# Performance work log

Measured on AMD Instinct MI355X. Metric: run time of the kernel, lower is better.

Reference implementation:

```python
import jax, jax.numpy as jnp
import numpy as np

TEMPERATURE = 8.0  # sqrt(d_k) with d_k=64

def setup_inputs() -> dict:
    key = jax.random.key(0)
    k1, k2, k3, k4 = jax.random.split(key, 4)
    B, L, D = 64, 1024, 64  # B = batch*n_heads
    q = jax.random.normal(k1, (B, L, D), dtype=jnp.float32)
    k = jax.random.normal(k2, (B, L, D), dtype=jnp.float32)
    v = jax.random.normal(k3, (B, L, D), dtype=jnp.float32)
    mask = jax.random.randint(k4, (B, L, L), 0, 2).astype(jnp.bool_)
    return {"q": q, "k": k, "v": v, "mask": mask}

def reference(q, k, v, mask):
    # scores: [B, Lq, Lk]
    attn = jnp.einsum('bqd,bkd->bqk', q, k) / TEMPERATURE
    attn = jnp.where(mask, -jnp.inf, attn)
    attn = jax.nn.softmax(attn, axis=2)
    output = jnp.einsum('bqk,bkd->bqd', attn, v)
    return (output, attn)
```

## Files before the change

kernel.cpp:

```cpp
#include <hip/hip_runtime.h>

#define B_ 64
#define L_ 1024
#define D_ 64
#define QT 16

typedef _Float16 f16;
typedef __attribute__((ext_vector_type(8))) _Float16 f16x8;
typedef __attribute__((ext_vector_type(4))) _Float16 f16x4;
typedef __attribute__((ext_vector_type(4))) float f32x4;
typedef unsigned long long u64;
typedef unsigned long long u64x4 __attribute__((ext_vector_type(4)));

#define WS_KH 0u
#define WS_VT 8388608u
#define WS_BT 16777216u
#define WS_NEED 25165824u

#define MFMA32(A, B, C) __builtin_amdgcn_mfma_f32_16x16x32_f16((A), (B), (C), 0, 0, 0)
#define PV16(A, B, C)   __builtin_amdgcn_mfma_f32_16x16x16f16((A), (B), (C), 0, 0, 0)

__global__ __launch_bounds__(256)
void mega_prep(const float* __restrict__ kk, const float* __restrict__ v,
               const unsigned char* __restrict__ mask,
               f16* __restrict__ kh, f16* __restrict__ vt, u64* __restrict__ bits) {
    __shared__ f16 tile[64][72];
    const int bid = blockIdx.x;
    if (bid < 2048) {
        const int i = (bid * 256 + threadIdx.x) * 8;
        float4 f0 = *(const float4*)(kk + i);
        float4 f1 = *(const float4*)(kk + i + 4);
        float fv[8] = {f0.x, f0.y, f0.z, f0.w, f1.x, f1.y, f1.z, f1.w};
        f16x8 h;
        #pragma unroll
        for (int j = 0; j < 8; ++j) h[j] = (f16)(fv[j] * 0.125f);
        *(f16x8*)(kh + i) = h;
    } else if (bid < 3072) {
        const int bb = bid - 2048;
        const int b = bb >> 4, kt = bb & 15;
        const int r = threadIdx.x >> 2, c0 = (threadIdx.x & 3) * 16;
        const float* vp = v + (size_t)(b * L_ + kt * 64 + r) * D_ + c0;
        float4 g0 = *(const float4*)vp;
        float4 g1 = *(const float4*)(vp + 4);
        float4 g2 = *(const float4*)(vp + 8);
        float4 g3 = *(const float4*)(vp + 12);
        float fv[16] = {g0.x, g0.y, g0.z, g0.w, g1.x, g1.y, g1.z, g1.w,
                        g2.x, g2.y, g2.z, g2.w, g3.x, g3.y, g3.z, g3.w};
        #pragma unroll
        for (int j = 0; j < 16; ++j) tile[r][c0 + j] = (f16)fv[j];
        __syncthreads();
        f16x8 o0, o1;
        #pragma unroll
        for (int j = 0; j < 8; ++j) { o0[j] = tile[c0 + j][r]; o1[j] = tile[c0 + 8 + j][r]; }
        f16* op = vt + (size_t)(b * 64 + r) * 1024 + kt * 64 + c0;
        *(f16x8*)op = o0;
        *(f16x8*)(op + 8) = o1;
    } else {
        unsigned det = 0;
        {
            const unsigned* mw = (const unsigned*)mask;
            #pragma unroll
            for (int i = 0; i < 32; ++i) det |= mw[i];
        }
        const bool elem4 = (det <= 1u) || (det == 0x3F800000u);
        const int lane = threadIdx.x & 63;
        const int gw = (bid - 3072) * 4 + (threadIdx.x >> 6);
        for (int s = gw; s < 262144; s += 8192) {
            unsigned nib;
            if (elem4) {
                const int4 m = *(const int4*)((const int*)mask + (size_t)s * 256 + lane * 4);
                nib = (m.x != 0 ? 1u : 0u) | (m.y != 0 ? 2u : 0u) |
                      (m.z != 0 ? 4u : 0u) | (m.w != 0 ? 8u : 0u);
            } else {
                const uchar4 m = *(const uchar4*)(mask + (size_t)s * 256 + lane * 4);
                nib = (m.x ? 1u : 0u) | (m.y ? 2u : 0u) | (m.z ? 4u : 0u) | (m.w ? 8u : 0u);
            }
            u64 b0 = __ballot((nib & 1u) != 0u);
            u64 b1 = __ballot((nib & 2u) != 0u);
            u64 b2 = __ballot((nib & 4u) != 0u);
            u64 b3 = __ballot((nib & 8u) != 0u);
            if (lane == 0) {
                u64x4 o = {b0, b1, b2, b3};
                *(u64x4*)(bits + (size_t)s * 4) = o;
            }
        }
    }
}


__global__ __launch_bounds__(256, 4)
void sdpa_main(const float* __restrict__ q, const f16* __restrict__ kh,
               const f16* __restrict__ vt, const u64* __restrict__ bits,
               float* __restrict__ out, float* __restrict__ attn)
{
    const int tid = threadIdx.x;
    const int l = tid & 63, w = tid >> 6;
    const int lr = l & 15, lg = l >> 4;
    const int bid0 = blockIdx.x;
    const int bid = (bid0 & 7) * 128 + (bid0 >> 3);
    const int tile_id = bid * 4 + w;
    const int b = tile_id >> 6;
    const int qbase = tile_id * QT;

    f16x8 aq0, aq1;
    {
        const float* qp = q + (size_t)(qbase + lr) * D_;
        float4 f0 = *(const float4*)(qp + lg * 8);
        float4 f1 = *(const float4*)(qp + lg * 8 + 4);
        float4 f2 = *(const float4*)(qp + 32 + lg * 8);
        float4 f3 = *(const float4*)(qp + 32 + lg * 8 + 4);
        aq0[0] = (f16)f0.x; aq0[1] = (f16)f0.y; aq0[2] = (f16)f0.z; aq0[3] = (f16)f0.w;
        aq0[4] = (f16)f1.x; aq0[5] = (f16)f1.y; aq0[6] = (f16)f1.z; aq0[7] = (f16)f1.w;
        aq1[0] = (f16)f2.x; aq1[1] = (f16)f2.y; aq1[2] = (f16)f2.z; aq1[3] = (f16)f2.w;
        aq1[4] = (f16)f3.x; aq1[5] = (f16)f3.y; aq1[6] = (f16)f3.z; aq1[7] = (f16)f3.w;
    }

    const f16* khb = kh + (size_t)b * (L_ * D_) + lg * 8;
    const f16* vtb = vt + (size_t)b * (D_ * L_);
    const u64x4* bp = (const u64x4*)bits + (size_t)(qbase + lr) * 4;

    float rsum = 0.f;
    f16x8 kc0, kc1;
    {
        const f16* kp = khb + (size_t)lr * D_;
        kc0 = *(const f16x8*)kp;
        kc1 = *(const f16x8*)(kp + 32);
    }
    #pragma unroll
    for (int sp = 0; sp < 4; ++sp) {
        const u64x4 bw = bp[sp];
        #pragma unroll 4
        for (int cc = 0; cc < 16; ++cc) {
            const int c = sp * 16 + cc;
            f16x8 kn0, kn1;
            if (c < 63) {
                const f16* kp = khb + (size_t)((c + 1) * 16 + lr) * D_;
                kn0 = *(const f16x8*)kp;
                kn1 = *(const f16x8*)(kp + 32);
            }
            f32x4 s = {0.f, 0.f, 0.f, 0.f};
            s = MFMA32(kc0, aq0, s);
            s = MFMA32(kc1, aq1, s);
            const int sh = cc * 4 + lg;
            rsum += ((unsigned)(bw[0] >> sh) & 1u) ? 0.f : __expf(s[0]);
            rsum += ((unsigned)(bw[1] >> sh) & 1u) ? 0.f : __expf(s[1]);
            rsum += ((unsigned)(bw[2] >> sh) & 1u) ? 0.f : __expf(s[2]);
            rsum += ((unsigned)(bw[3] >> sh) & 1u) ? 0.f : __expf(s[3]);
            kc0 = kn0; kc1 = kn1;
        }
    }
    rsum += __shfl_xor(rsum, 16);
    rsum += __shfl_xor(rsum, 32);
    const float inv = 1.0f / rsum;

    f32x4 o0 = {0.f,0.f,0.f,0.f}, o1 = {0.f,0.f,0.f,0.f};
    f32x4 o2 = {0.f,0.f,0.f,0.f}, o3 = {0.f,0.f,0.f,0.f};
    {
        const f16* kp = khb + (size_t)lr * D_;
        kc0 = *(const f16x8*)kp;
        kc1 = *(const f16x8*)(kp + 32);
    }
    float* ap = attn + (size_t)(qbase + lr) * L_ + lg * 4;
    const f16* vpb = vtb + (size_t)lr * L_ + lg * 4;
    #pragma unroll
    for (int sp = 0; sp < 4; ++sp) {
        const u64x4 bw = bp[sp];
        #pragma unroll 4
        for (int cc = 0; cc < 16; ++cc) {
            const int c = sp * 16 + cc;
            f16x8 kn0, kn1;
            if (c < 63) {
                const f16* kp = khb + (size_t)((c + 1) * 16 + lr) * D_;
                kn0 = *(const f16x8*)kp;
                kn1 = *(const f16x8*)(kp + 32);
            }
            f32x4 s = {0.f, 0.f, 0.f, 0.f};
            s = MFMA32(kc0, aq0, s);
            s = MFMA32(kc1, aq1, s);
            const int sh = cc * 4 + lg;
            f32x4 p;
            p[0] = (((unsigned)(bw[0] >> sh) & 1u) ? 0.f : __expf(s[0])) * inv;
            p[1] = (((unsigned)(bw[1] >> sh) & 1u) ? 0.f : __expf(s[1])) * inv;
            p[2] = (((unsigned)(bw[2] >> sh) & 1u) ? 0.f : __expf(s[2])) * inv;
            p[3] = (((unsigned)(bw[3] >> sh) & 1u) ? 0.f : __expf(s[3])) * inv;
            *(f32x4*)(ap + c * 16) = p;
            f16x4 pa;
            pa[0] = (f16)p[0]; pa[1] = (f16)p[1]; pa[2] = (f16)p[2]; pa[3] = (f16)p[3];
            const f16* vp = vpb + c * 16;
            f16x4 v0 = *(const f16x4*)vp;
            f16x4 v1 = *(const f16x4*)(vp + 16 * L_);
            f16x4 v2 = *(const f16x4*)(vp + 32 * L_);
            f16x4 v3 = *(const f16x4*)(vp + 48 * L_);
            o0 = PV16(pa, v0, o0);
            o1 = PV16(pa, v1, o1);
            o2 = PV16(pa, v2, o2);
            o3 = PV16(pa, v3, o3);
            kc0 = kn0; kc1 = kn1;
        }
    }

    float* op = out + (size_t)(qbase + lg * 4) * D_ + lr;
    #pragma unroll
    for (int r = 0; r < 4; ++r) {
        op[r * D_ + 0]  = o0[r];
        op[r * D_ + 16] = o1[r];
        op[r * D_ + 32] = o2[r];
        op[r * D_ + 48] = o3[r];
    }
}


__device__ __forceinline__ int sidx(int row, int col) {
    return row * 1024 + ((((col >> 3) ^ (row & 7)) << 3) | (col & 7));
}

__global__ __launch_bounds__(256, 4)
void sdpa_fallback(const float* __restrict__ q, const float* __restrict__ kk,
                   const float* __restrict__ v, const unsigned char* __restrict__ mask,
                   float* __restrict__ out, float* __restrict__ attn)
{
    __shared__ f16 S[QT * 1024];
    __shared__ float wmax[4][QT];
    __shared__ float wsum[QT];

    const int tid = threadIdx.x;
    const int l = tid & 63, w = tid >> 6;
    const int lr = l & 15, lg = l >> 4;
    const int bid = blockIdx.x;
    const int b = bid >> 6, qt = bid & 63;
    const int qbase = b * L_ + qt * QT;

    unsigned det = 0;
    {
        const unsigned* mw = (const unsigned*)mask;
        #pragma unroll
        for (int i = 0; i < 32; ++i) det |= mw[i];
    }
    const bool elem4 = (det <= 1u) || (det == 0x3F800000u);

    f16x8 aqh[2], aql[2];
    {
        const float* qp = q + (size_t)(qbase + lr) * D_;
        #pragma unroll
        for (int s = 0; s < 2; ++s) {
            float4 f0 = *(const float4*)(qp + s * 32 + lg * 8);
            float4 f1 = *(const float4*)(qp + s * 32 + lg * 8 + 4);
            float fv[8] = {f0.x, f0.y, f0.z, f0.w, f1.x, f1.y, f1.z, f1.w};
            #pragma unroll
            for (int j = 0; j < 8; ++j) {
                f16 h = (f16)fv[j];
                aqh[s][j] = h;
                aql[s][j] = (f16)(fv[j] - (float)h);
            }
        }
    }

    float vmax[4] = {-INFINITY, -INFINITY, -INFINITY, -INFINITY};
    const float* kb = kk + (size_t)(b * L_ + w * 16 + lr) * D_ + lg * 8;
    const size_t mrowbase = (size_t)(qbase + lg * 4) * L_ + w * 16 + lr;

    float4 kc[4];
    kc[0] = *(const float4*)kb;
    kc[1] = *(const float4*)(kb + 4);
    kc[2] = *(const float4*)(kb + 32);
    kc[3] = *(const float4*)(kb + 36);
    int mcur[4], mnxt[4];
    #pragma unroll
    for (int r2 = 0; r2 < 4; ++r2) {
        if (elem4) {
            mcur[r2] = ((const int*)mask)[mrowbase + (size_t)r2 * L_];
            mnxt[r2] = ((const int*)mask)[mrowbase + (size_t)r2 * L_ + 64];
        } else {
            mcur[r2] = mask[mrowbase + (size_t)r2 * L_];
            mnxt[r2] = mask[mrowbase + (size_t)r2 * L_ + 64];
        }
    }

    for (int ck = 0; ck < 16; ++ck) {
        float4 kn[4];
        if (ck < 15) {
            const float* kp = kb + (size_t)(ck + 1) * 64 * D_;
            kn[0] = *(const float4*)kp;
            kn[1] = *(const float4*)(kp + 4);
            kn[2] = *(const float4*)(kp + 32);
            kn[3] = *(const float4*)(kp + 36);
        }
        int mfut[4];
        if (ck < 14) {
            const size_t mo = mrowbase + (size_t)(ck + 2) * 64;
            if (elem4) {
                #pragma unroll
                for (int r2 = 0; r2 < 4; ++r2) mfut[r2] = ((const int*)mask)[mo + (size_t)r2 * L_];
            } else {
                #pragma unroll
                for (int r2 = 0; r2 < 4; ++r2) mfut[r2] = mask[mo + (size_t)r2 * L_];
            }
        }
        f16x8 bh[2], bl[2];
        #pragma unroll
        for (int s = 0; s < 2; ++s) {
            float fv[8] = {kc[2*s].x, kc[2*s].y, kc[2*s].z, kc[2*s].w,
                           kc[2*s+1].x, kc[2*s+1].y, kc[2*s+1].z, kc[2*s+1].w};
            #pragma unroll
            for (int j = 0; j < 8; ++j) {
                f16 h = (f16)fv[j];
                bh[s][j] = h;
                bl[s][j] = (f16)(fv[j] - (float)h);
            }
        }
        f32x4 acc = {0.f, 0.f, 0.f, 0.f};
        #pragma unroll
        for (int s = 0; s < 2; ++s) {
            acc = MFMA32(aqh[s], bh[s], acc);
            acc = MFMA32(aql[s], bh[s], acc);
            acc = MFMA32(aqh[s], bl[s], acc);
        }
        const int scol = ck * 64 + w * 16 + lr;
        #pragma unroll
        for (int r2 = 0; r2 < 4; ++r2) {
            float sv = mcur[r2] ? -INFINITY : acc[r2] * 0.125f;
            S[sidx(lg * 4 + r2, scol)] = (f16)sv;
            vmax[r2] = fmaxf(vmax[r2], sv);
        }
        #pragma unroll
        for (int r2 = 0; r2 < 4; ++r2) mcur[r2] = mnxt[r2];
        if (ck < 14) {
            #pragma unroll
            for (int r2 = 0; r2 < 4; ++r2) mnxt[r2] = mfut[r2];
        }
        if (ck < 15) {
            #pragma unroll
            for (int j = 0; j < 4; ++j) kc[j] = kn[j];
        }
    }
    #pragma unroll
    for (int r2 = 0; r2 < 4; ++r2) {
        #pragma unroll
        for (int off = 1; off < 16; off <<= 1)
            vmax[r2] = fmaxf(vmax[r2], __shfl_xor(vmax[r2], off));
    }
    if (lr == 0) {
        #pragma unroll
        for (int r2 = 0; r2 < 4; ++r2) wmax[w][lg * 4 + r2] = vmax[r2];
    }
    __syncthreads();

    {
        const int row = tid >> 4, cg = tid & 15;
        const float m = fmaxf(fmaxf(wmax[0][row], wmax[1][row]),
                              fmaxf(wmax[2][row], wmax[3][row]));
        float sum = 0.f;
        #pragma unroll
        for (int c = 0; c < 8; ++c) {
            f16* sp = &S[row * 1024 + (((cg + 16 * c) ^ (row & 7)) << 3)];
            f16x8 sv = *(const f16x8*)sp;
            f16x8 evv;
            #pragma unroll
            for (int j = 0; j < 8; ++j) {
                float e = __expf((float)sv[j] - m);
                evv[j] = (f16)e;
                sum += e;
            }
            *(f16x8*)sp = evv;
        }
        #pragma unroll
        for (int off = 1; off < 16; off <<= 1) sum += __shfl_xor(sum, off);
        if (cg == 0) wsum[row] = sum;
        __syncthreads();

        const float inv = 1.0f / wsum[row];
        float* ap = attn + (size_t)(qbase + row) * L_;
        #pragma unroll
        for (int c = 0; c < 8; ++c) {
            f16x8 evv = *(const f16x8*)&S[row * 1024 + (((cg + 16 * c) ^ (row & 7)) << 3)];
            float4 p0, p1;
            p0.x = (float)evv[0] * inv; p0.y = (float)evv[1] * inv;
            p0.z = (float)evv[2] * inv; p0.w = (float)evv[3] * inv;
            p1.x = (float)evv[4] * inv; p1.y = (float)evv[5] * inv;
            p1.z = (float)evv[6] * inv; p1.w = (float)evv[7] * inv;
            *(float4*)(ap + (cg + 16 * c) * 8)     = p0;
            *(float4*)(ap + (cg + 16 * c) * 8 + 4) = p1;
        }
    }

    f32x4 acc2 = {0.f, 0.f, 0.f, 0.f};
    const float* vb = v + (size_t)(b * L_) * D_ + w * 16 + lr;
    float vcA[8], vcB[8];
    #pragma unroll
    for (int j = 0; j < 8; ++j) {
        vcA[j] = vb[(size_t)(lg * 8 + j) * D_];
        vcB[j] = vb[(size_t)(32 + lg * 8 + j) * D_];
    }
    for (int tt = 0; tt < 16; ++tt) {
        {
            f16x8 pa = *(const f16x8*)&S[lr * 1024 + ((((2 * tt) * 4 + lg) ^ (lr & 7)) << 3)];
            f16x8 bv;
            #pragma unroll
            for (int j = 0; j < 8; ++j) bv[j] = (f16)vcA[j];
            if (tt < 15) {
                const float* vp = vb + (size_t)((2 * tt + 2) * 32 + lg * 8) * D_;
                #pragma unroll
                for (int j = 0; j < 8; ++j) vcA[j] = vp[(size_t)j * D_];
            }
            acc2 = MFMA32(pa, bv, acc2);
        }
        {
            f16x8 pa = *(const f16x8*)&S[lr * 1024 + ((((2 * tt + 1) * 4 + lg) ^ (lr & 7)) << 3)];
            f16x8 bv;
            #pragma unroll
            for (int j = 0; j < 8; ++j) bv[j] = (f16)vcB[j];
            if (tt < 15) {
                const float* vp = vb + (size_t)((2 * tt + 3) * 32 + lg * 8) * D_;
                #pragma unroll
                for (int j = 0; j < 8; ++j) vcB[j] = vp[(size_t)j * D_];
            }
            acc2 = MFMA32(pa, bv, acc2);
        }
    }

    #pragma unroll
    for (int r2 = 0; r2 < 4; ++r2) {
        const float invr = 1.0f / wsum[lg * 4 + r2];
        out[(size_t)(qbase + lg * 4 + r2) * D_ + w * 16 + lr] = acc2[r2] * invr;
    }
}

extern "C" void kernel_launch(void* const* d_in, const int* in_sizes, int n_in,
                              void* d_out, int out_size, void* d_ws, size_t ws_size,
                              hipStream_t stream) {
    const float* q = (const float*)d_in[0];
    const float* k = (const float*)d_in[1];
    const float* v = (const float*)d_in[2];
    const unsigned char* mask = (const unsigned char*)d_in[3];
    float* out = (float*)d_out;
    float* attn = out + (size_t)B_ * L_ * D_;

    if (ws_size >= (size_t)WS_NEED) {
        f16* kh = (f16*)((char*)d_ws + WS_KH);
        f16* vt = (f16*)((char*)d_ws + WS_VT);
        u64* bits = (u64*)((char*)d_ws + WS_BT);
        mega_prep<<<dim3(5120), 256, 0, stream>>>(k, v, mask, kh, vt, bits);
        sdpa_main<<<dim3(1024), 256, 0, stream>>>(q, kh, vt, bits, out, attn);
    } else {
        sdpa_fallback<<<dim3(B_ * (L_ / QT)), 256, 0, stream>>>(q, k, v, mask, out, attn);
    }
}
```

Before: 328.9 us.

## Pre-pack K/V in MFMA fragment order and stage attn writes through LDS

The prep kernel now writes K and V in per-lane MFMA fragment order, so the main kernel loads each fragment with one contiguous coalesced read per 16-key chunk. V fragments are prefetched one chunk ahead, the same way K already was. The attention probabilities are stored as f16 in a swizzled LDS buffer and then written to attn as full coalesced rows, replacing the strided per-lane float4 stores. This adds 32KB of shared memory per block and lowers the launch bound to 3 blocks per CU. The attn output now holds f16-rounded probabilities instead of fp32 values, which loses some precision.

```diff
diff --git a/kernel.cpp b/kernel.cpp
--- a/kernel.cpp
+++ b/kernel.cpp
@@ -12,8 +12,8 @@
 typedef unsigned long long u64;
 typedef unsigned long long u64x4 __attribute__((ext_vector_type(4)));
 
-#define WS_KH 0u
-#define WS_VT 8388608u
+#define WS_KP 0u
+#define WS_VP 8388608u
 #define WS_BT 16777216u
 #define WS_NEED 25165824u
 
@@ -23,18 +23,24 @@
 __global__ __launch_bounds__(256)
 void mega_prep(const float* __restrict__ kk, const float* __restrict__ v,
                const unsigned char* __restrict__ mask,
-               f16* __restrict__ kh, f16* __restrict__ vt, u64* __restrict__ bits) {
+               f16* __restrict__ kpack, f16* __restrict__ vpack, u64* __restrict__ bits) {
     __shared__ f16 tile[64][72];
     const int bid = blockIdx.x;
+    const int l = threadIdx.x & 63;
+    const int lr = l & 15, lg = l >> 4;
     if (bid < 2048) {
-        const int i = (bid * 256 + threadIdx.x) * 8;
-        float4 f0 = *(const float4*)(kk + i);
-        float4 f1 = *(const float4*)(kk + i + 4);
-        float fv[8] = {f0.x, f0.y, f0.z, f0.w, f1.x, f1.y, f1.z, f1.w};
-        f16x8 h;
-        #pragma unroll
-        for (int j = 0; j < 8; ++j) h[j] = (f16)(fv[j] * 0.125f);
-        *(f16x8*)(kh + i) = h;
+        const int gw = bid * 4 + (threadIdx.x >> 6);
+        const int b = gw >> 7, wid = gw & 127;
+        const int c = wid >> 1, h = wid & 1;
+        const float* kp = kk + ((size_t)(b * L_ + c * 16 + lr)) * D_ + h * 32 + lg * 8;
+        float4 f0 = *(const float4*)kp;
+        float4 f1 = *(const float4*)(kp + 4);
+        f16x8 o;
+        o[0] = (f16)(f0.x * 0.125f); o[1] = (f16)(f0.y * 0.125f);
+        o[2] = (f16)(f0.z * 0.125f); o[3] = (f16)(f0.w * 0.125f);
+        o[4] = (f16)(f1.x * 0.125f); o[5] = (f16)(f1.y * 0.125f);
+        o[6] = (f16)(f1.z * 0.125f); o[7] = (f16)(f1.w * 0.125f);
+        *(f16x8*)(kpack + (size_t)gw * 512 + l * 8) = o;
     } else if (bid < 3072) {
         const int bb = bid - 2048;
         const int b = bb >> 4, kt = bb & 15;
@@ -49,12 +55,16 @@
         #pragma unroll
         for (int j = 0; j < 16; ++j) tile[r][c0 + j] = (f16)fv[j];
         __syncthreads();
-        f16x8 o0, o1;
-        #pragma unroll
-        for (int j = 0; j < 8; ++j) { o0[j] = tile[c0 + j][r]; o1[j] = tile[c0 + 8 + j][r]; }
-        f16* op = vt + (size_t)(b * 64 + r) * 1024 + kt * 64 + c0;
-        *(f16x8*)op = o0;
-        *(f16x8*)(op + 8) = o1;
+        const int cl = threadIdx.x >> 6;
+        const int c = kt * 4 + cl;
+        #pragma unroll
+        for (int nt = 0; nt < 4; ++nt) {
+            f16x4 o;
+            #pragma unroll
+            for (int j = 0; j < 4; ++j)
+                o[j] = tile[cl * 16 + lg * 4 + j][nt * 16 + lr];
+            *(f16x4*)(vpack + (size_t)b * 65536 + c * 1024 + nt * 256 + l * 4) = o;
+        }
     } else {
         unsigned det = 0;
         {
@@ -63,23 +73,22 @@
             for (int i = 0; i < 32; ++i) det |= mw[i];
         }
         const bool elem4 = (det <= 1u) || (det == 0x3F800000u);
-        const int lane = threadIdx.x & 63;
         const int gw = (bid - 3072) * 4 + (threadIdx.x >> 6);
         for (int s = gw; s < 262144; s += 8192) {
             unsigned nib;
             if (elem4) {
-                const int4 m = *(const int4*)((const int*)mask + (size_t)s * 256 + lane * 4);
+                const int4 m = *(const int4*)((const int*)mask + (size_t)s * 256 + l * 4);
                 nib = (m.x != 0 ? 1u : 0u) | (m.y != 0 ? 2u : 0u) |
                       (m.z != 0 ? 4u : 0u) | (m.w != 0 ? 8u : 0u);
             } else {
-                const uchar4 m = *(const uchar4*)(mask + (size_t)s * 256 + lane * 4);
+                const uchar4 m = *(const uchar4*)(mask + (size_t)s * 256 + l * 4);
                 nib = (m.x ? 1u : 0u) | (m.y ? 2u : 0u) | (m.z ? 4u : 0u) | (m.w ? 8u : 0u);
             }
             u64 b0 = __ballot((nib & 1u) != 0u);
             u64 b1 = __ballot((nib & 2u) != 0u);
             u64 b2 = __ballot((nib & 4u) != 0u);
             u64 b3 = __ballot((nib & 8u) != 0u);
-            if (lane == 0) {
+            if (l == 0) {
                 u64x4 o = {b0, b1, b2, b3};
                 *(u64x4*)(bits + (size_t)s * 4) = o;
             }
@@ -88,11 +97,12 @@
 }
 
 
-__global__ __launch_bounds__(256, 4)
-void sdpa_main(const float* __restrict__ q, const f16* __restrict__ kh,
-               const f16* __restrict__ vt, const u64* __restrict__ bits,
+__global__ __launch_bounds__(256, 3)
+void sdpa_main(const float* __restrict__ q, const f16* __restrict__ kpack,
+               const f16* __restrict__ vpack, const u64* __restrict__ bits,
                float* __restrict__ out, float* __restrict__ attn)
 {
+    __shared__ f16 SL[4 * 4096];
     const int tid = threadIdx.x;
     const int l = tid & 63, w = tid >> 6;
     const int lr = l & 15, lg = l >> 4;
@@ -115,28 +125,23 @@
         aq1[4] = (f16)f3.x; aq1[5] = (f16)f3.y; aq1[6] = (f16)f3.z; aq1[7] = (f16)f3.w;
     }
 
-    const f16* khb = kh + (size_t)b * (L_ * D_) + lg * 8;
-    const f16* vtb = vt + (size_t)b * (D_ * L_);
+    const f16* kpb = kpack + (size_t)b * 65536;
+    const f16* vpb = vpack + (size_t)b * 65536;
     const u64x4* bp = (const u64x4*)bits + (size_t)(qbase + lr) * 4;
 
     float rsum = 0.f;
-    f16x8 kc0, kc1;
-    {
-        const f16* kp = khb + (size_t)lr * D_;
-        kc0 = *(const f16x8*)kp;
-        kc1 = *(const f16x8*)(kp + 32);
-    }
+    f16x8 kc0 = *(const f16x8*)(kpb + l * 8);
+    f16x8 kc1 = *(const f16x8*)(kpb + 512 + l * 8);
     #pragma unroll
     for (int sp = 0; sp < 4; ++sp) {
         const u64x4 bw = bp[sp];
-        #pragma unroll 4
+        #pragma unroll
         for (int cc = 0; cc < 16; ++cc) {
             const int c = sp * 16 + cc;
             f16x8 kn0, kn1;
             if (c < 63) {
-                const f16* kp = khb + (size_t)((c + 1) * 16 + lr) * D_;
-                kn0 = *(const f16x8*)kp;
-                kn1 = *(const f16x8*)(kp + 32);
+                kn0 = *(const f16x8*)(kpb + (c + 1) * 1024 + l * 8);
+                kn1 = *(const f16x8*)(kpb + (c + 1) * 1024 + 512 + l * 8);
             }
             f32x4 s = {0.f, 0.f, 0.f, 0.f};
             s = MFMA32(kc0, aq0, s);
@@ -155,48 +160,57 @@
 
     f32x4 o0 = {0.f,0.f,0.f,0.f}, o1 = {0.f,0.f,0.f,0.f};
     f32x4 o2 = {0.f,0.f,0.f,0.f}, o3 = {0.f,0.f,0.f,0.f};
-    {
-        const f16* kp = khb + (size_t)lr * D_;
-        kc0 = *(const f16x8*)kp;
-        kc1 = *(const f16x8*)(kp + 32);
-    }
-    float* ap = attn + (size_t)(qbase + lr) * L_ + lg * 4;
-    const f16* vpb = vtb + (size_t)lr * L_ + lg * 4;
+    kc0 = *(const f16x8*)(kpb + l * 8);
+    kc1 = *(const f16x8*)(kpb + 512 + l * 8);
+    f16x4 bv0 = *(const f16x4*)(vpb + l * 4);
+    f16x4 bv1 = *(const f16x4*)(vpb + 256 + l * 4);
+    f16x4 bv2 = *(const f16x4*)(vpb + 512 + l * 4);
+    f16x4 bv3 = *(const f16x4*)(vpb + 768 + l * 4);
+    f16* slw = SL + w * 4096;
+    const int swz = (lr & 15) << 2;
     #pragma unroll
     for (int sp = 0; sp < 4; ++sp) {
         const u64x4 bw = bp[sp];
-        #pragma unroll 4
+        #pragma unroll
         for (int cc = 0; cc < 16; ++cc) {
             const int c = sp * 16 + cc;
             f16x8 kn0, kn1;
+            f16x4 bn0, bn1, bn2, bn3;
             if (c < 63) {
-                const f16* kp = khb + (size_t)((c + 1) * 16 + lr) * D_;
-                kn0 = *(const f16x8*)kp;
-                kn1 = *(const f16x8*)(kp + 32);
+                kn0 = *(const f16x8*)(kpb + (c + 1) * 1024 + l * 8);
+                kn1 = *(const f16x8*)(kpb + (c + 1) * 1024 + 512 + l * 8);
+                bn0 = *(const f16x4*)(vpb + (c + 1) * 1024 + l * 4);
+                bn1 = *(const f16x4*)(vpb + (c + 1) * 1024 + 256 + l * 4);
+                bn2 = *(const f16x4*)(vpb + (c + 1) * 1024 + 512 + l * 4);
+                bn3 = *(const f16x4*)(vpb + (c + 1) * 1024 + 768 + l * 4);
             }
             f32x4 s = {0.f, 0.f, 0.f, 0.f};
             s = MFMA32(kc0, aq0, s);
             s = MFMA32(kc1, aq1, s);
             const int sh = cc * 4 + lg;
-            f32x4 p;
-            p[0] = (((unsigned)(bw[0] >> sh) & 1u) ? 0.f : __expf(s[0])) * inv;
-            p[1] = (((unsigned)(bw[1] >> sh) & 1u) ? 0.f : __expf(s[1])) * inv;
-            p[2] = (((unsigned)(bw[2] >> sh) & 1u) ? 0.f : __expf(s[2])) * inv;
-            p[3] = (((unsigned)(bw[3] >> sh) & 1u) ? 0.f : __expf(s[3])) * inv;
-            *(f32x4*)(ap + c * 16) = p;
             f16x4 pa;
-            pa[0] = (f16)p[0]; pa[1] = (f16)p[1]; pa[2] = (f16)p[2]; pa[3] = (f16)p[3];
-            const f16* vp = vpb + c * 16;
-            f16x4 v0 = *(const f16x4*)vp;
-            f16x4 v1 = *(const f16x4*)(vp + 16 * L_);
-            f16x4 v2 = *(const f16x4*)(vp + 32 * L_);
-            f16x4 v3 = *(const f16x4*)(vp + 48 * L_);
-            o0 = PV16(pa, v0, o0);
-            o1 = PV16(pa, v1, o1);
-            o2 = PV16(pa, v2, o2);
-            o3 = PV16(pa, v3, o3);
+            pa[0] = (f16)((((unsigned)(bw[0] >> sh) & 1u) ? 0.f : __expf(s[0])) * inv);
+            pa[1] = (f16)((((unsigned)(bw[1] >> sh) & 1u) ? 0.f : __expf(s[1])) * inv);
+            pa[2] = (f16)((((unsigned)(bw[2] >> sh) & 1u) ? 0.f : __expf(s[2])) * inv);
+            pa[3] = (f16)((((unsigned)(bw[3] >> sh) & 1u) ? 0.f : __expf(s[3])) * inv);
+            *(f16x4*)&slw[lr * 256 + ((cc * 16 + lg * 4) ^ swz)] = pa;
+            o0 = PV16(pa, bv0, o0);
+            o1 = PV16(pa, bv1, o1);
+            o2 = PV16(pa, bv2, o2);
+            o3 = PV16(pa, bv3, o3);
             kc0 = kn0; kc1 = kn1;
-        }
+            bv0 = bn0; bv1 = bn1; bv2 = bn2; bv3 = bn3;
+        }
+        asm volatile("s_waitcnt lgkmcnt(0)" ::: "memory");
+        __builtin_amdgcn_sched_barrier(0);
+        #pragma unroll
+        for (int r0 = 0; r0 < 16; ++r0) {
+            f16x4 pv = *(const f16x4*)&slw[r0 * 256 + ((l * 4) ^ ((r0 & 15) << 2))];
+            f32x4 pf = {(float)pv[0], (float)pv[1], (float)pv[2], (float)pv[3]};
+            *(f32x4*)(attn + (size_t)(qbase + r0) * L_ + sp * 256 + l * 4) = pf;
+        }
+        asm volatile("s_waitcnt lgkmcnt(0)" ::: "memory");
+        __builtin_amdgcn_sched_barrier(0);
     }
 
     float* op = out + (size_t)(qbase + lg * 4) * D_ + lr;
@@ -436,11 +450,11 @@
     float* attn = out + (size_t)B_ * L_ * D_;
 
     if (ws_size >= (size_t)WS_NEED) {
-        f16* kh = (f16*)((char*)d_ws + WS_KH);
-        f16* vt = (f16*)((char*)d_ws + WS_VT);
+        f16* kpack = (f16*)((char*)d_ws + WS_KP);
+        f16* vpack = (f16*)((char*)d_ws + WS_VP);
         u64* bits = (u64*)((char*)d_ws + WS_BT);
-        mega_prep<<<dim3(5120), 256, 0, stream>>>(k, v, mask, kh, vt, bits);
-        sdpa_main<<<dim3(1024), 256, 0, stream>>>(q, kh, vt, bits, out, attn);
+        mega_prep<<<dim3(5120), 256, 0, stream>>>(k, v, mask, kpack, vpack, bits);
+        sdpa_main<<<dim3(1024), 256, 0, stream>>>(q, kpack, vpack, bits, out, attn);
     } else {
         sdpa_fallback<<<dim3(B_ * (L_ / QT)), 256, 0, stream>>>(q, k, v, mask, out, attn);
     }
```

Result: faster. 300.7 us (-8.6%).
